# Kernel optimization log

Measured on AMD Instinct MI355X. Metric: run time of the kernel, lower is better.

## Reference

```python
import jax, jax.numpy as jnp
import numpy as np
from jax import lax

PAD = 960          # tf.pad amount each side
LN_EPS = 1e-3      # keras LayerNormalization default epsilon


def _process(x, h, gamma, beta):
    """SmallConvNet: grouped 1D conv (per-channel learnable kernel) -> LayerNorm -> SiLU.
    x: (B, 2, 64), h: (2, 961) -> (B, 2, 1024). Dropout omitted (see notes)."""
    # grouped conv: each of the 2 'sequence' channels has its own length-961 kernel
    y = lax.conv_general_dilated(
        x, h[:, None, :],                 # kernel (O=2, I=1, W=961)
        window_strides=(1,), padding=[(PAD, PAD)],
        dimension_numbers=("NCH", "OIH", "NCH"),
        feature_group_count=2)            # (B, 2, 1024)
    mu = jnp.mean(y, axis=-1, keepdims=True)
    var = jnp.mean(jnp.square(y - mu), axis=-1, keepdims=True)
    ln = gamma * (y - mu) * lax.rsqrt(var + LN_EPS) + beta
    return jax.nn.silu(ln)


def reference(values, h, gamma, beta, symbols):
    # values: (B, 2, 64); symbols: (2, 64)
    vp = _process(values, h, gamma, beta)                              # (B, 2, 1024)
    sp = _process(jnp.zeros_like(values) + symbols, h, gamma, beta)    # (B, 2, 1024)
    # sign-based cosine-similarity attention: S[b,i,j] = mean_d sign(vp[b,j,d])*sign(vp[b,j,d]+sp[b,i,d])
    Xi = vp[:, None, :, :]   # (B, 1, N, D)
    Xj = sp[:, :, None, :]   # (B, N, 1, D)
    S = jnp.mean(jnp.sign(Xi) * jnp.sign(Xi + Xj), axis=-1)           # (B, N, N)
    scores = jax.nn.softmax(S, axis=-1)
    attn = jnp.einsum("bij,bjd->bid", scores, vp)                     # (B, N, D)
    return jax.nn.silu(attn * sp)


def setup_inputs() -> dict:
    key = jax.random.key(0)
    k1, k2, k3 = jax.random.split(key, 3)
    B, N, Din, D = 16384, 2, 64, 1024
    return {
        "values": jax.random.normal(k1, (B, N, Din), dtype=jnp.float32),
        "h": jax.random.normal(k2, (2, 961), dtype=jnp.float32),
        "gamma": jnp.ones((D,), dtype=jnp.float32),
        "beta": jnp.zeros((D,), dtype=jnp.float32),
        "symbols": jax.random.normal(k3, (N, Din), dtype=jnp.float32),
    }
```

## Files before the change

kernel.cpp:

```cpp
#include <hip/hip_runtime.h>

#define LN_EPS 1e-3f

typedef __attribute__((ext_vector_type(8))) short bf16x8;
typedef __attribute__((ext_vector_type(4))) float f32x4;

static __device__ __forceinline__ float sgnf(float x) {
    return (x > 0.f) ? 1.f : ((x < 0.f) ? -1.f : 0.f);
}
static __device__ __forceinline__ float siluf(float x) { return x / (1.f + __expf(-x)); }

static __device__ __forceinline__ unsigned short f2bf(float f) {
    unsigned int u = __float_as_uint(f);
    return (unsigned short)((u + 0x7fffu + ((u >> 16) & 1u)) >> 16);
}
static __device__ __forceinline__ float bf2f(unsigned short s) {
    return __uint_as_float(((unsigned int)s) << 16);
}
static __device__ __forceinline__ void split3(float v, unsigned short& hi,
                                              unsigned short& mid, unsigned short& lo) {
    hi = f2bf(v);
    const float r1 = v - bf2f(hi);
    mid = f2bf(r1);
    const float r2 = r1 - bf2f(mid);
    lo = f2bf(r2);
}

#define SPOFF 196608

__global__ __launch_bounds__(256) void hd_prep_sp(
    const float* __restrict__ h, const float* __restrict__ symbols,
    const float* __restrict__ gamma, const float* __restrict__ beta,
    float* __restrict__ ws)
{
    __shared__ float h_pad[2][1088];
    __shared__ float x_s[2][64];
    __shared__ float red[4][2];
    const int t = threadIdx.x;

    for (int idx = t; idx < 2 * 1088; idx += 256) {
        const int c = idx / 1088, j = idx - c * 1088;
        float v = 0.f;
        if (j >= 63 && j <= 1023) v = h[c * 961 + (j - 63)];
        h_pad[c][j] = v;
    }
    if (t < 128) x_s[t >> 6][t & 63] = symbols[t];
    __syncthreads();

    const int c = t >> 7, tt = t & 127;
    const int lane = t & 63, wid = t >> 6;
    const int jbase = 1023 - tt;

    float acc[8];
    #pragma unroll
    for (int k = 0; k < 8; ++k) acc[k] = 0.f;

    #pragma unroll 8
    for (int i = 0; i < 64; ++i) {
        const float xv = x_s[c][i];
        #pragma unroll
        for (int k = 0; k < 8; ++k)
            acc[k] = fmaf(xv, h_pad[c][jbase + i - 128 * k], acc[k]);
    }

    float ps = 0.f, pq = 0.f;
    #pragma unroll
    for (int k = 0; k < 8; ++k) { ps += acc[k]; pq += acc[k] * acc[k]; }
    #pragma unroll
    for (int off = 32; off; off >>= 1) {
        ps += __shfl_xor(ps, off);
        pq += __shfl_xor(pq, off);
    }
    if (lane == 0) { red[wid][0] = ps; red[wid][1] = pq; }
    __syncthreads();

    const float sum = red[2 * c][0] + red[2 * c + 1][0];
    const float sq  = red[2 * c][1] + red[2 * c + 1][1];
    const float mu  = sum * (1.f / 1024.f);
    float var = sq * (1.f / 1024.f) - mu * mu;
    var = fmaxf(var, 0.f);
    const float rs = rsqrtf(var + LN_EPS);

    #pragma unroll
    for (int k = 0; k < 8; ++k) {
        const int d = tt + 128 * k;
        const float ln = (acc[k] - mu) * rs * gamma[d] + beta[d];
        ws[SPOFF + c * 1024 + d] = siluf(ln);
    }
}

__global__ __launch_bounds__(256) void hd_prep_bpack(
    const float* __restrict__ h, float* __restrict__ ws)
{
    unsigned short* Bp = (unsigned short*)ws;
    const int total = 2 * 2 * 64 * 64 * 8;
    for (int e = blockIdx.x * 256 + threadIdx.x; e < total; e += gridDim.x * 256) {
        const int j   = e & 7;
        const int l   = (e >> 3) & 63;
        const int ntg = (e >> 9) & 63;
        const int ks  = (e >> 15) & 1;
        const int c   = (e >> 16) & 1;
        const int H = 1023 - (16 * ntg + (l & 15)) + 32 * ks + 8 * (l >> 4) + j;
        float v = 0.f;
        if (H >= 63 && H <= 1023) v = h[c * 961 + (H - 63)];
        unsigned short hi, mid, lo;
        split3(v, hi, mid, lo);
        const int base = ((((c * 2 + ks) * 64 + ntg) * 64 + l) * 3) * 8 + j;
        Bp[base]      = hi;
        Bp[base + 8]  = mid;
        Bp[base + 16] = lo;
    }
}

__global__ __launch_bounds__(256, 2) void hd_main_mfma(
    const float* __restrict__ values,
    const float* __restrict__ gamma, const float* __restrict__ beta,
    const float* __restrict__ ws, float* __restrict__ out)
{
    __shared__ float stats[4][4][2][4][2];
    __shared__ int   sred [4][4][2][4][2];
    __shared__ float otile[4][4][264];

    const int t = threadIdx.x;
    const int w = t >> 6, l = t & 63;
    const int g = l >> 4, q = l & 15;
    const int b0 = blockIdx.x * 16;

    bf16x8 ahi[2][2], amd_[2][2], alo[2][2];
    #pragma unroll
    for (int c = 0; c < 2; ++c) {
        #pragma unroll
        for (int ks = 0; ks < 2; ++ks) {
            const float* xp = values + ((size_t)(b0 + q) * 2 + c) * 64 + ks * 32 + g * 8;
            const float4 x0 = *reinterpret_cast<const float4*>(xp);
            const float4 x1 = *reinterpret_cast<const float4*>(xp + 4);
            const float xv[8] = {x0.x, x0.y, x0.z, x0.w, x1.x, x1.y, x1.z, x1.w};
            bf16x8 h8, m8, l8;
            #pragma unroll
            for (int j = 0; j < 8; ++j) {
                unsigned short hb, mb, lb;
                split3(xv[j], hb, mb, lb);
                h8[j] = (short)hb;
                m8[j] = (short)mb;
                l8[j] = (short)lb;
            }
            ahi[c][ks] = h8;
            amd_[c][ks] = m8;
            alo[c][ks] = l8;
        }
    }

    const bf16x8* Bv = reinterpret_cast<const bf16x8*>(ws) + (size_t)l * 3;
    f32x4 acc[2][16];
    #pragma unroll
    for (int c = 0; c < 2; ++c)
        #pragma unroll
        for (int nt = 0; nt < 16; ++nt)
            acc[c][nt] = (f32x4){0.f, 0.f, 0.f, 0.f};

    #pragma unroll
    for (int nt = 0; nt < 16; ++nt) {
        const int ntg = w * 16 + nt;
        #pragma unroll
        for (int c = 0; c < 2; ++c) {
            f32x4 ts = {0.f, 0.f, 0.f, 0.f};
            f32x4 tm = {0.f, 0.f, 0.f, 0.f};
            f32x4 th = {0.f, 0.f, 0.f, 0.f};
            #pragma unroll
            for (int ks = 0; ks < 2; ++ks) {
                const bf16x8* p = Bv + (size_t)((c * 2 + ks) * 64 + ntg) * 192;
                const bf16x8 bh = p[0], bm = p[1], bl = p[2];
                ts = __builtin_amdgcn_mfma_f32_16x16x32_bf16(amd_[c][ks], bl, ts, 0, 0, 0);
                ts = __builtin_amdgcn_mfma_f32_16x16x32_bf16(alo[c][ks], bm, ts, 0, 0, 0);
                ts = __builtin_amdgcn_mfma_f32_16x16x32_bf16(ahi[c][ks], bl, ts, 0, 0, 0);
                ts = __builtin_amdgcn_mfma_f32_16x16x32_bf16(amd_[c][ks], bm, ts, 0, 0, 0);
                ts = __builtin_amdgcn_mfma_f32_16x16x32_bf16(alo[c][ks], bh, ts, 0, 0, 0);
                tm = __builtin_amdgcn_mfma_f32_16x16x32_bf16(ahi[c][ks], bm, tm, 0, 0, 0);
                tm = __builtin_amdgcn_mfma_f32_16x16x32_bf16(amd_[c][ks], bh, tm, 0, 0, 0);
                th = __builtin_amdgcn_mfma_f32_16x16x32_bf16(ahi[c][ks], bh, th, 0, 0, 0);
            }
            #pragma unroll
            for (int r = 0; r < 4; ++r)
                acc[c][nt][r] = (ts[r] + tm[r]) + th[r];
        }
    }

    {
        float s_[2][4], q_[2][4];
        #pragma unroll
        for (int c = 0; c < 2; ++c)
            #pragma unroll
            for (int r = 0; r < 4; ++r) { s_[c][r] = 0.f; q_[c][r] = 0.f; }
        #pragma unroll
        for (int c = 0; c < 2; ++c)
            #pragma unroll
            for (int nt = 0; nt < 16; ++nt)
                #pragma unroll
                for (int r = 0; r < 4; ++r) {
                    const float v = acc[c][nt][r];
                    s_[c][r] += v;
                    q_[c][r] += v * v;
                }
        #pragma unroll
        for (int off = 1; off < 16; off <<= 1)
            #pragma unroll
            for (int c = 0; c < 2; ++c)
                #pragma unroll
                for (int r = 0; r < 4; ++r) {
                    s_[c][r] += __shfl_xor(s_[c][r], off);
                    q_[c][r] += __shfl_xor(q_[c][r], off);
                }
        if (q == 0) {
            #pragma unroll
            for (int c = 0; c < 2; ++c)
                #pragma unroll
                for (int r = 0; r < 4; ++r) {
                    stats[w][g][c][r][0] = s_[c][r];
                    stats[w][g][c][r][1] = q_[c][r];
                }
        }
    }
    __syncthreads();

    float mu_[2][4], rs_[2][4];
    #pragma unroll
    for (int c = 0; c < 2; ++c)
        #pragma unroll
        for (int r = 0; r < 4; ++r) {
            float S = 0.f, Q = 0.f;
            #pragma unroll
            for (int w2 = 0; w2 < 4; ++w2) {
                S += stats[w2][g][c][r][0];
                Q += stats[w2][g][c][r][1];
            }
            const float mu = S * (1.f / 1024.f);
            float var = Q * (1.f / 1024.f) - mu * mu;
            var = fmaxf(var, 0.f);
            mu_[c][r] = mu;
            rs_[c][r] = rsqrtf(var + LN_EPS);
        }

    const int dbase = w * 256 + q;
    #pragma unroll
    for (int nt = 0; nt < 16; ++nt) {
        const int d = dbase + 16 * nt;
        const float gam = gamma[d];
        const float bet = beta[d];
        #pragma unroll
        for (int c = 0; c < 2; ++c)
            #pragma unroll
            for (int r = 0; r < 4; ++r)
                acc[c][nt][r] = siluf((acc[c][nt][r] - mu_[c][r]) * rs_[c][r] * gam + bet);
    }

    int cnt[2][4][2];
    #pragma unroll
    for (int c = 0; c < 2; ++c)
        #pragma unroll
        for (int r = 0; r < 4; ++r) { cnt[c][r][0] = 0; cnt[c][r][1] = 0; }
    #pragma unroll
    for (int nt = 0; nt < 16; ++nt) {
        const int d = dbase + 16 * nt;
        const float sp0 = ws[SPOFF + d];
        const float sp1 = ws[SPOFF + 1024 + d];
        #pragma unroll
        for (int c = 0; c < 2; ++c)
            #pragma unroll
            for (int r = 0; r < 4; ++r) {
                const float v = acc[c][nt][r];
                const unsigned int iv = __float_as_uint(v);
                cnt[c][r][0] += (int)((iv ^ __float_as_uint(v + sp0)) >> 31);
                cnt[c][r][1] += (int)((iv ^ __float_as_uint(v + sp1)) >> 31);
            }
    }
    #pragma unroll
    for (int off = 1; off < 16; off <<= 1)
        #pragma unroll
        for (int c = 0; c < 2; ++c)
            #pragma unroll
            for (int r = 0; r < 4; ++r) {
                cnt[c][r][0] += __shfl_xor(cnt[c][r][0], off);
                cnt[c][r][1] += __shfl_xor(cnt[c][r][1], off);
            }
    if (q == 0) {
        #pragma unroll
        for (int c = 0; c < 2; ++c)
            #pragma unroll
            for (int r = 0; r < 4; ++r) {
                sred[w][g][c][r][0] = cnt[c][r][0];
                sred[w][g][c][r][1] = cnt[c][r][1];
            }
    }
    __syncthreads();

    float p0_[4][2], p1_[4][2];
    #pragma unroll
    for (int r = 0; r < 4; ++r)
        #pragma unroll
        for (int a = 0; a < 2; ++a) {
            int t0 = 0, t1 = 0;
            #pragma unroll
            for (int w2 = 0; w2 < 4; ++w2) {
                t0 += sred[w2][g][0][r][a];
                t1 += sred[w2][g][1][r][a];
            }
            const float S0 = 1.f - 2.f * (float)t0 * (1.f / 1024.f);
            const float S1 = 1.f - 2.f * (float)t1 * (1.f / 1024.f);
            const float m  = fmaxf(S0, S1);
            const float e0 = __expf(S0 - m), e1 = __expf(S1 - m);
            const float inv = 1.f / (e0 + e1);
            p0_[r][a] = e0 * inv;
            p1_[r][a] = e1 * inv;
        }

    #pragma unroll
    for (int a = 0; a < 2; ++a) {
        #pragma unroll
        for (int r = 0; r < 4; ++r) {
            #pragma unroll
            for (int nt = 0; nt < 16; ++nt) {
                const int d = dbase + 16 * nt;
                const float spa = ws[SPOFF + a * 1024 + d];
                const float attn = p0_[r][a] * acc[0][nt][r] + p1_[r][a] * acc[1][nt][r];
                otile[w][g][16 * nt + q] = siluf(attn * spa);
            }
            __syncthreads();
            #pragma unroll
            for (int g2 = 0; g2 < 4; ++g2) {
                const float4 v4 = *reinterpret_cast<const float4*>(&otile[w][g2][4 * l]);
                *reinterpret_cast<float4*>(
                    out + ((size_t)(b0 + 4 * g2 + r) * 2 + a) * 1024 + 256 * w + 4 * l) = v4;
            }
            __syncthreads();
        }
    }
}

__global__ __launch_bounds__(256) void hd_prep_scalar(
    const float* __restrict__ h, const float* __restrict__ symbols,
    const float* __restrict__ gamma, const float* __restrict__ beta,
    float* __restrict__ ws)
{
    __shared__ float h_pad[2][1088];
    __shared__ float x_s[2][64];
    __shared__ float red[4][2];
    const int t = threadIdx.x;

    for (int idx = t; idx < 2 * 1088; idx += 256) {
        const int c = idx / 1088, j = idx - c * 1088;
        float v = 0.f;
        if (j >= 63 && j <= 1023) v = h[c * 961 + (j - 63)];
        h_pad[c][j] = v;
        const int src = 1086 - j;
        float vr = 0.f;
        if (src >= 63 && src <= 1023) vr = h[c * 961 + (src - 63)];
        ws[c * 1088 + j] = vr;
    }
    if (t < 128) x_s[t >> 6][t & 63] = symbols[t];
    __syncthreads();

    const int c = t >> 7, tt = t & 127;
    const int lane = t & 63, wid = t >> 6;
    const int jbase = 1023 - tt;

    float acc[8];
    #pragma unroll
    for (int k = 0; k < 8; ++k) acc[k] = 0.f;

    #pragma unroll 8
    for (int i = 0; i < 64; ++i) {
        const float xv = x_s[c][i];
        #pragma unroll
        for (int k = 0; k < 8; ++k)
            acc[k] = fmaf(xv, h_pad[c][jbase + i - 128 * k], acc[k]);
    }

    float ps = 0.f, pq = 0.f;
    #pragma unroll
    for (int k = 0; k < 8; ++k) { ps += acc[k]; pq += acc[k] * acc[k]; }
    #pragma unroll
    for (int off = 32; off; off >>= 1) {
        ps += __shfl_xor(ps, off);
        pq += __shfl_xor(pq, off);
    }
    if (lane == 0) { red[wid][0] = ps; red[wid][1] = pq; }
    __syncthreads();

    const float sum = red[2 * c][0] + red[2 * c + 1][0];
    const float sq  = red[2 * c][1] + red[2 * c + 1][1];
    const float mu  = sum * (1.f / 1024.f);
    float var = sq * (1.f / 1024.f) - mu * mu;
    var = fmaxf(var, 0.f);
    const float rs = rsqrtf(var + LN_EPS);

    #pragma unroll
    for (int k = 0; k < 8; ++k) {
        const int d = tt + 128 * k;
        const float ln = (acc[k] - mu) * rs * gamma[d] + beta[d];
        ws[2176 + c * 1024 + d] = siluf(ln);
    }
}

__global__ __launch_bounds__(256, 4) void hd_main_scalar(
    const float* __restrict__ values,
    const float* __restrict__ gamma, const float* __restrict__ beta,
    const float* __restrict__ ws, float* __restrict__ out)
{
    __shared__ float hrev[2][1088];
    __shared__ float red[4][16];
    __shared__ float redf[16];
    __shared__ float red2[4][16];
    __shared__ float redf2[16];

    const int t = threadIdx.x;
    const int lane = t & 63, wid = t >> 6;
    const size_t b0 = (size_t)blockIdx.x * 4;

    for (int idx = t; idx < 2 * 1088; idx += 256)
        (&hrev[0][0])[idx] = ws[idx];
    __syncthreads();

    float acc[4][2][4];
    #pragma unroll
    for (int b = 0; b < 4; ++b)
        #pragma unroll
        for (int c = 0; c < 2; ++c)
            #pragma unroll
            for (int k = 0; k < 4; ++k) acc[b][c][k] = 0.f;

    #pragma unroll 1
    for (int i0 = 0; i0 < 64; i0 += 8) {
        const int q0 = 56 + 4 * t - i0;
        float r[2][12];
        #pragma unroll
        for (int c = 0; c < 2; ++c) {
            const float4* p = reinterpret_cast<const float4*>(&hrev[c][q0]);
            const float4 a0 = p[0], a1 = p[1], a2 = p[2];
            r[c][0] = a0.x; r[c][1] = a0.y; r[c][2]  = a0.z; r[c][3]  = a0.w;
            r[c][4] = a1.x; r[c][5] = a1.y; r[c][6]  = a1.z; r[c][7]  = a1.w;
            r[c][8] = a2.x; r[c][9] = a2.y; r[c][10] = a2.z; r[c][11] = a2.w;
        }
        #pragma unroll
        for (int b = 0; b < 4; ++b) {
            #pragma unroll
            for (int c = 0; c < 2; ++c) {
                const float* xp = values + ((b0 + b) * 2 + c) * 64 + i0;
                #pragma unroll
                for (int il = 0; il < 8; ++il) {
                    const float xv = xp[il];
                    #pragma unroll
                    for (int k = 0; k < 4; ++k)
                        acc[b][c][k] = fmaf(xv, r[c][7 - il + k], acc[b][c][k]);
                }
            }
        }
    }

    {
        float v16[16];
        #pragma unroll
        for (int b = 0; b < 4; ++b)
            #pragma unroll
            for (int c = 0; c < 2; ++c) {
                const float a0 = acc[b][c][0], a1 = acc[b][c][1];
                const float a2 = acc[b][c][2], a3 = acc[b][c][3];
                v16[(b * 2 + c) * 2]     = a0 + a1 + a2 + a3;
                v16[(b * 2 + c) * 2 + 1] = a0 * a0 + a1 * a1 + a2 * a2 + a3 * a3;
            }
        #pragma unroll
        for (int off = 32; off; off >>= 1)
            #pragma unroll
            for (int v = 0; v < 16; ++v)
                v16[v] += __shfl_xor(v16[v], off);
        if (lane == 0) {
            #pragma unroll
            for (int v = 0; v < 16; ++v) red[wid][v] = v16[v];
        }
    }
    __syncthreads();
    if (t < 16) redf[t] = red[0][t] + red[1][t] + red[2][t] + red[3][t];
    __syncthreads();

    const float4 g4  = *reinterpret_cast<const float4*>(&gamma[4 * t]);
    const float4 be4 = *reinterpret_cast<const float4*>(&beta[4 * t]);
    float sp_r[2][4];
    #pragma unroll
    for (int a = 0; a < 2; ++a) {
        const float4 s4 = *reinterpret_cast<const float4*>(&ws[2176 + a * 1024 + 4 * t]);
        sp_r[a][0] = s4.x; sp_r[a][1] = s4.y; sp_r[a][2] = s4.z; sp_r[a][3] = s4.w;
    }
    const float gk[4] = {g4.x, g4.y, g4.z, g4.w};
    const float bk[4] = {be4.x, be4.y, be4.z, be4.w};

    #pragma unroll
    for (int b = 0; b < 4; ++b)
        #pragma unroll
        for (int c = 0; c < 2; ++c) {
            const float sum = redf[(b * 2 + c) * 2];
            const float sq  = redf[(b * 2 + c) * 2 + 1];
            const float mu  = sum * (1.f / 1024.f);
            float var = sq * (1.f / 1024.f) - mu * mu;
            var = fmaxf(var, 0.f);
            const float rs = rsqrtf(var + LN_EPS);
            #pragma unroll
            for (int k = 0; k < 4; ++k)
                acc[b][c][k] = siluf((acc[b][c][k] - mu) * rs * gk[k] + bk[k]);
        }

    {
        float v16[16];
        #pragma unroll
        for (int b = 0; b < 4; ++b)
            #pragma unroll
            for (int a = 0; a < 2; ++a)
                #pragma unroll
                for (int c = 0; c < 2; ++c) {
                    float s = 0.f;
                    #pragma unroll
                    for (int k = 0; k < 4; ++k)
                        s += sgnf(acc[b][c][k]) * sgnf(acc[b][c][k] + sp_r[a][k]);
                    v16[b * 4 + a * 2 + c] = s;
                }
        #pragma unroll
        for (int off = 32; off; off >>= 1)
            #pragma unroll
            for (int v = 0; v < 16; ++v)
                v16[v] += __shfl_xor(v16[v], off);
        if (lane == 0) {
            #pragma unroll
            for (int v = 0; v < 16; ++v) red2[wid][v] = v16[v];
        }
    }
    __syncthreads();
    if (t < 16) redf2[t] = red2[0][t] + red2[1][t] + red2[2][t] + red2[3][t];
    __syncthreads();

    #pragma unroll
    for (int b = 0; b < 4; ++b) {
        #pragma unroll
        for (int a = 0; a < 2; ++a) {
            const float s0 = redf2[b * 4 + a * 2 + 0] * (1.f / 1024.f);
            const float s1 = redf2[b * 4 + a * 2 + 1] * (1.f / 1024.f);
            const float m  = fmaxf(s0, s1);
            const float e0 = __expf(s0 - m), e1 = __expf(s1 - m);
            const float inv = 1.f / (e0 + e1);
            const float p0 = e0 * inv, p1 = e1 * inv;
            float4 o;
            o.x = siluf((p0 * acc[b][0][0] + p1 * acc[b][1][0]) * sp_r[a][0]);
            o.y = siluf((p0 * acc[b][0][1] + p1 * acc[b][1][1]) * sp_r[a][1]);
            o.z = siluf((p0 * acc[b][0][2] + p1 * acc[b][1][2]) * sp_r[a][2]);
            o.w = siluf((p0 * acc[b][0][3] + p1 * acc[b][1][3]) * sp_r[a][3]);
            *reinterpret_cast<float4*>(out + ((b0 + b) * 2 + a) * 1024 + 4 * t) = o;
        }
    }
}

extern "C" void kernel_launch(void* const* d_in, const int* in_sizes, int n_in,
                              void* d_out, int out_size, void* d_ws, size_t ws_size,
                              hipStream_t stream) {
    const float* values  = (const float*)d_in[0];
    const float* h       = (const float*)d_in[1];
    const float* gamma   = (const float*)d_in[2];
    const float* beta    = (const float*)d_in[3];
    const float* symbols = (const float*)d_in[4];
    float* out = (float*)d_out;
    float* ws  = (float*)d_ws;

    const int B = in_sizes[0] / 128;

    if (ws_size >= 794624) {
        hipLaunchKernelGGL(hd_prep_sp, dim3(1), dim3(256), 0, stream,
                           h, symbols, gamma, beta, ws);
        hipLaunchKernelGGL(hd_prep_bpack, dim3(256), dim3(256), 0, stream, h, ws);
        hipLaunchKernelGGL(hd_main_mfma, dim3(B / 16), dim3(256), 0, stream,
                           values, gamma, beta, ws, out);
    } else {
        hipLaunchKernelGGL(hd_prep_scalar, dim3(1), dim3(256), 0, stream,
                           h, symbols, gamma, beta, ws);
        hipLaunchKernelGGL(hd_main_scalar, dim3(B / 4), dim3(256), 0, stream,
                           values, gamma, beta, ws, out);
    }
}
```

Before: 130.1 us.

## Split MFMA main kernel across 16 waves per block with planar B packing

Raises the main kernel block from 4 to 16 wavefronts, so each wave computes 4 output column tiles instead of 16. This cuts per-thread accumulator registers and spreads the work of each 16-row batch across more waves. The packed B operand is laid out as separate hi/mid/lo planes so lane loads are contiguous, and a second reduction stage over 16 waves is added for the LayerNorm stats and the sign counts. The cost is extra barriers, scalar rather than float4 output stores, and each block's A fragments being converted redundantly by 4x more waves.

```diff
diff --git a/kernel.cpp b/kernel.cpp
--- a/kernel.cpp
+++ b/kernel.cpp
@@ -105,21 +105,23 @@
         if (H >= 63 && H <= 1023) v = h[c * 961 + (H - 63)];
         unsigned short hi, mid, lo;
         split3(v, hi, mid, lo);
-        const int base = ((((c * 2 + ks) * 64 + ntg) * 64 + l) * 3) * 8 + j;
-        Bp[base]      = hi;
-        Bp[base + 8]  = mid;
-        Bp[base + 16] = lo;
-    }
-}
-
-__global__ __launch_bounds__(256, 2) void hd_main_mfma(
+        const int T = (c * 2 + ks) * 64 + ntg;
+        Bp[((T * 192 +   0 + l)) * 8 + j] = hi;
+        Bp[((T * 192 +  64 + l)) * 8 + j] = mid;
+        Bp[((T * 192 + 128 + l)) * 8 + j] = lo;
+    }
+}
+
+__global__ __launch_bounds__(1024, 4) void hd_main_mfma(
     const float* __restrict__ values,
     const float* __restrict__ gamma, const float* __restrict__ beta,
     const float* __restrict__ ws, float* __restrict__ out)
 {
-    __shared__ float stats[4][4][2][4][2];
-    __shared__ int   sred [4][4][2][4][2];
-    __shared__ float otile[4][4][264];
+    __shared__ float stats[16][4][2][4][2];
+    __shared__ int   sred [16][4][2][4][2];
+    __shared__ float statsF[64];
+    __shared__ int   sredF [64];
+    __shared__ float otile[16][4][72];
 
     const int t = threadIdx.x;
     const int w = t >> 6, l = t & 63;
@@ -150,17 +152,17 @@
         }
     }
 
-    const bf16x8* Bv = reinterpret_cast<const bf16x8*>(ws) + (size_t)l * 3;
-    f32x4 acc[2][16];
+    const bf16x8* Bv = reinterpret_cast<const bf16x8*>(ws) + l;
+    f32x4 acc[2][4];
     #pragma unroll
     for (int c = 0; c < 2; ++c)
         #pragma unroll
-        for (int nt = 0; nt < 16; ++nt)
+        for (int nt = 0; nt < 4; ++nt)
             acc[c][nt] = (f32x4){0.f, 0.f, 0.f, 0.f};
 
     #pragma unroll
-    for (int nt = 0; nt < 16; ++nt) {
-        const int ntg = w * 16 + nt;
+    for (int nt = 0; nt < 4; ++nt) {
+        const int ntg = w * 4 + nt;
         #pragma unroll
         for (int c = 0; c < 2; ++c) {
             f32x4 ts = {0.f, 0.f, 0.f, 0.f};
@@ -169,7 +171,7 @@
             #pragma unroll
             for (int ks = 0; ks < 2; ++ks) {
                 const bf16x8* p = Bv + (size_t)((c * 2 + ks) * 64 + ntg) * 192;
-                const bf16x8 bh = p[0], bm = p[1], bl = p[2];
+                const bf16x8 bh = p[0], bm = p[64], bl = p[128];
                 ts = __builtin_amdgcn_mfma_f32_16x16x32_bf16(amd_[c][ks], bl, ts, 0, 0, 0);
                 ts = __builtin_amdgcn_mfma_f32_16x16x32_bf16(alo[c][ks], bm, ts, 0, 0, 0);
                 ts = __builtin_amdgcn_mfma_f32_16x16x32_bf16(ahi[c][ks], bl, ts, 0, 0, 0);
@@ -194,7 +196,7 @@
         #pragma unroll
         for (int c = 0; c < 2; ++c)
             #pragma unroll
-            for (int nt = 0; nt < 16; ++nt)
+            for (int nt = 0; nt < 4; ++nt)
                 #pragma unroll
                 for (int r = 0; r < 4; ++r) {
                     const float v = acc[c][nt][r];
@@ -221,18 +223,22 @@
         }
     }
     __syncthreads();
+    if (t < 64) {
+        const int gg = t >> 4, cc = (t >> 3) & 1, rr = (t >> 1) & 3, ss = t & 1;
+        float S = 0.f;
+        #pragma unroll
+        for (int w2 = 0; w2 < 16; ++w2) S += stats[w2][gg][cc][rr][ss];
+        statsF[t] = S;
+    }
+    __syncthreads();
 
     float mu_[2][4], rs_[2][4];
     #pragma unroll
     for (int c = 0; c < 2; ++c)
         #pragma unroll
         for (int r = 0; r < 4; ++r) {
-            float S = 0.f, Q = 0.f;
-            #pragma unroll
-            for (int w2 = 0; w2 < 4; ++w2) {
-                S += stats[w2][g][c][r][0];
-                Q += stats[w2][g][c][r][1];
-            }
+            const float S = statsF[((g * 2 + c) * 4 + r) * 2 + 0];
+            const float Q = statsF[((g * 2 + c) * 4 + r) * 2 + 1];
             const float mu = S * (1.f / 1024.f);
             float var = Q * (1.f / 1024.f) - mu * mu;
             var = fmaxf(var, 0.f);
@@ -240,9 +246,9 @@
             rs_[c][r] = rsqrtf(var + LN_EPS);
         }
 
-    const int dbase = w * 256 + q;
-    #pragma unroll
-    for (int nt = 0; nt < 16; ++nt) {
+    const int dbase = w * 64 + q;
+    #pragma unroll
+    for (int nt = 0; nt < 4; ++nt) {
         const int d = dbase + 16 * nt;
         const float gam = gamma[d];
         const float bet = beta[d];
@@ -259,7 +265,7 @@
         #pragma unroll
         for (int r = 0; r < 4; ++r) { cnt[c][r][0] = 0; cnt[c][r][1] = 0; }
     #pragma unroll
-    for (int nt = 0; nt < 16; ++nt) {
+    for (int nt = 0; nt < 4; ++nt) {
         const int d = dbase + 16 * nt;
         const float sp0 = ws[SPOFF + d];
         const float sp1 = ws[SPOFF + 1024 + d];
@@ -292,18 +298,22 @@
             }
     }
     __syncthreads();
+    if (t < 64) {
+        const int gg = t >> 4, cc = (t >> 3) & 1, rr = (t >> 1) & 3, aa = t & 1;
+        int S = 0;
+        #pragma unroll
+        for (int w2 = 0; w2 < 16; ++w2) S += sred[w2][gg][cc][rr][aa];
+        sredF[t] = S;
+    }
+    __syncthreads();
 
     float p0_[4][2], p1_[4][2];
     #pragma unroll
     for (int r = 0; r < 4; ++r)
         #pragma unroll
         for (int a = 0; a < 2; ++a) {
-            int t0 = 0, t1 = 0;
-            #pragma unroll
-            for (int w2 = 0; w2 < 4; ++w2) {
-                t0 += sred[w2][g][0][r][a];
-                t1 += sred[w2][g][1][r][a];
-            }
+            const int t0 = sredF[((g * 2 + 0) * 4 + r) * 2 + a];
+            const int t1 = sredF[((g * 2 + 1) * 4 + r) * 2 + a];
             const float S0 = 1.f - 2.f * (float)t0 * (1.f / 1024.f);
             const float S1 = 1.f - 2.f * (float)t1 * (1.f / 1024.f);
             const float m  = fmaxf(S0, S1);
@@ -318,7 +328,7 @@
         #pragma unroll
         for (int r = 0; r < 4; ++r) {
             #pragma unroll
-            for (int nt = 0; nt < 16; ++nt) {
+            for (int nt = 0; nt < 4; ++nt) {
                 const int d = dbase + 16 * nt;
                 const float spa = ws[SPOFF + a * 1024 + d];
                 const float attn = p0_[r][a] * acc[0][nt][r] + p1_[r][a] * acc[1][nt][r];
@@ -327,9 +337,8 @@
             __syncthreads();
             #pragma unroll
             for (int g2 = 0; g2 < 4; ++g2) {
-                const float4 v4 = *reinterpret_cast<const float4*>(&otile[w][g2][4 * l]);
-                *reinterpret_cast<float4*>(
-                    out + ((size_t)(b0 + 4 * g2 + r) * 2 + a) * 1024 + 256 * w + 4 * l) = v4;
+                const float v1 = otile[w][g2][l];
+                out[((size_t)(b0 + 4 * g2 + r) * 2 + a) * 1024 + 64 * w + l] = v1;
             }
             __syncthreads();
         }
@@ -572,7 +581,7 @@
         hipLaunchKernelGGL(hd_prep_sp, dim3(1), dim3(256), 0, stream,
                            h, symbols, gamma, beta, ws);
         hipLaunchKernelGGL(hd_prep_bpack, dim3(256), dim3(256), 0, stream, h, ws);
-        hipLaunchKernelGGL(hd_main_mfma, dim3(B / 16), dim3(256), 0, stream,
+        hipLaunchKernelGGL(hd_main_mfma, dim3(B / 16), dim3(1024), 0, stream,
                            values, gamma, beta, ws, out);
     } else {
         hipLaunchKernelGGL(hd_prep_scalar, dim3(1), dim3(256), 0, stream,
```

Measured after the change: 136.8 us. 5.1% more time.
